# Performance work log

Hardware: AMD Instinct MI355X
Metric: run time of the kernel (lower is better)

The kernel has to match this reference:

```python
import jax, jax.numpy as jnp
import numpy as np

B, T = 2, 512
D, H, DFF = 1024, 16, 4096
V, CSL = 32000, 16
NL, NDL = 4, 2
MAXLEN = 1024
DH = D // H


def generate_ar_mask(L, csl):
    m = np.zeros((2 * L, 2 * L), dtype=bool)
    for i in range(L):
        m[:i] = True
        m[L + (i // csl) * csl: L + i] = True
    return jnp.asarray(m)


def generate_block_ntp_mask(L, csl):
    m = np.zeros((2 * L, 2 * L), dtype=bool)
    for c in range(L // csl):
        if c - 1 >= 0:
            m[:(c - 1) * csl] = True
        m[L + c * csl: L + (c + 1) * csl] = True
    return jnp.asarray(m)


def layernorm(x, g, b, eps=1e-5):
    mu = x.mean(-1, keepdims=True)
    var = x.var(-1, keepdims=True)
    return (x - mu) / jnp.sqrt(var + eps) * g + b


def block(x, mask, p):
    ln1g, ln1b, wqkv, bqkv, wo, bo, ln2g, ln2b, w1, b1, w2, b2 = p
    h = layernorm(x, ln1g, ln1b)
    qkv = h @ wqkv + bqkv                       # [B,S,3D]
    q, k, v = jnp.split(qkv, 3, axis=-1)
    bs, S, _ = x.shape
    q = q.reshape(bs, S, H, DH).transpose(0, 2, 1, 3)
    k = k.reshape(bs, S, H, DH).transpose(0, 2, 1, 3)
    v = v.reshape(bs, S, H, DH).transpose(0, 2, 1, 3)
    scores = jnp.einsum('bhqd,bhkd->bhqk', q, k) / jnp.sqrt(jnp.asarray(DH, x.dtype))
    scores = jnp.where(mask, scores, jnp.asarray(-1e9, x.dtype))
    attn = jax.nn.softmax(scores, axis=-1)
    o = jnp.einsum('bhqk,bhkd->bhqd', attn, v)
    o = o.transpose(0, 2, 1, 3).reshape(bs, S, D)
    x = x + (o @ wo + bo)
    h = layernorm(x, ln2g, ln2b)
    return x + (jax.nn.gelu(h @ w1 + b1, approximate=False) @ w2 + b2)


def setup_inputs():
    key = jax.random.key(0)
    ks = jax.random.split(key, 6)

    def pstack(k, n):
        kk = jax.random.split(k, 4)
        return dict(
            ln1g=jnp.ones((n, D)), ln1b=jnp.zeros((n, D)),
            wqkv=0.02 * jax.random.normal(kk[0], (n, D, 3 * D)), bqkv=jnp.zeros((n, 3 * D)),
            wo=0.02 * jax.random.normal(kk[1], (n, D, D)), bo=jnp.zeros((n, D)),
            ln2g=jnp.ones((n, D)), ln2b=jnp.zeros((n, D)),
            w1=0.02 * jax.random.normal(kk[2], (n, D, DFF)), b1=jnp.zeros((n, DFF)),
            w2=0.02 * jax.random.normal(kk[3], (n, DFF, D)), b2=jnp.zeros((n, D)))

    body = pstack(ks[0], NL)
    dec = pstack(ks[1], NDL)
    inp = {
        'tok_ids': jax.random.randint(ks[2], (B, T), 0, V),
        'tok_emb': 0.02 * jax.random.normal(ks[3], (V, D)),
        'pos_emb': 0.02 * jax.random.normal(ks[4], (MAXLEN, D)),
        'mask_tokens': 0.02 * jax.random.normal(ks[5], (1, CSL, D)),
    }
    for kname, vv in body.items():
        inp['b_' + kname] = vv
    for kname, vv in dec.items():
        inp['d_' + kname] = vv
    return inp


def reference(tok_ids, tok_emb, pos_emb, mask_tokens,
              b_ln1g, b_ln1b, b_wqkv, b_bqkv, b_wo, b_bo, b_ln2g, b_ln2b, b_w1, b_b1, b_w2, b_b2,
              d_ln1g, d_ln1b, d_wqkv, d_bqkv, d_wo, d_bo, d_ln2g, d_ln2b, d_w1, d_b1, d_w2, d_b2):
    Bq, Tq = tok_ids.shape
    pos = jnp.tile(jnp.arange(Tq), 2)            # pos ids repeated for both halves
    emb_pos = pos_emb[pos]                       # [2T, D], broadcast over batch
    mask_ids = jnp.tile(mask_tokens, (Bq, Tq // CSL, 1))
    x = jnp.concatenate([tok_emb[tok_ids], mask_ids], axis=1) + emb_pos[None]

    body_mask = generate_block_ntp_mask(Tq, CSL)
    bp = (b_ln1g, b_ln1b, b_wqkv, b_bqkv, b_wo, b_bo, b_ln2g, b_ln2b, b_w1, b_b1, b_w2, b_b2)
    for i in range(NL):
        x = block(x, body_mask, tuple(p[i] for p in bp))

    ar_mask = generate_ar_mask(Tq, CSL)
    dp = (d_ln1g, d_ln1b, d_wqkv, d_bqkv, d_wo, d_bo, d_ln2g, d_ln2b, d_w1, d_b1, d_w2, d_b2)
    for i in range(NDL):
        x = block(x, ar_mask, tuple(p[i] for p in dp))

    logits = (x @ tok_emb.T)[:, Tq + 1:, :]      # [B, T-1, V]
    tgt = tok_ids[:, :-1].reshape(-1)
    logits = logits.reshape(-1, V)
    logp = jax.nn.log_softmax(logits, axis=-1)
    loss = -jnp.take_along_axis(logp, tgt[:, None], axis=1).mean()
    return loss
```

## Files before the change

kernel.cpp:

```cpp
#include <hip/hip_runtime.h>
#include <hip/hip_bf16.h>
#include <math.h>

#define DD   1024
#define HHN  16
#define DHD  64
#define DFFN 4096
#define VV   32000
#define BBN  2
#define TTN  512
#define SSN  1024
#define NRN  2048

typedef __attribute__((ext_vector_type(8))) short short8;
typedef __attribute__((ext_vector_type(4))) float f32x4;

enum : long {
    LSTR    = 12582912,
    OFF_QKV = 0,
    OFF_WO  = 3145728,
    OFF_W1  = 4194304,
    OFF_W2  = 8388608
};

struct P24 { const float* p[24]; };

__device__ __forceinline__ unsigned short f2bf(float f) {
    __hip_bfloat16 h = __float2bfloat16(f);
    return __builtin_bit_cast(unsigned short, h);
}
__device__ __forceinline__ float bf2f(unsigned short u) {
    return __bfloat162float(__builtin_bit_cast(__hip_bfloat16, u));
}

__device__ __forceinline__ void glds16(const void* g, void* l) {
    __builtin_amdgcn_global_load_lds(
        (const __attribute__((address_space(1))) void*)g,
        (__attribute__((address_space(3))) void*)l,
        16, 0, 0);
}

__device__ __forceinline__ float blockReduceSum(float v) {
    __shared__ float sh[4];
    #pragma unroll
    for (int o = 1; o < 64; o <<= 1) v += __shfl_xor(v, o, 64);
    int lane = threadIdx.x & 63, wv = threadIdx.x >> 6;
    __syncthreads();
    if (lane == 0) sh[wv] = v;
    __syncthreads();
    return sh[0] + sh[1] + sh[2] + sh[3];
}

__global__ __launch_bounds__(256) void prep_k(P24 wp, unsigned short* __restrict__ wbf,
                                              const int* __restrict__ tok,
                                              const float* __restrict__ temb,
                                              const float* __restrict__ pemb,
                                              const float* __restrict__ mtok,
                                              float* __restrict__ x) {
    __shared__ __align__(16) unsigned short Lb[256 * 72];
    const int id = blockIdx.x;
    const int t = threadIdx.x;

    if (id < 4608) {
        int seg, base, K, N;
        long woff;
        if (id < 1152)      { seg = 0; base = 0;    K = DD;   N = 3 * DD; woff = OFF_QKV; }
        else if (id < 1536) { seg = 1; base = 1152; K = DD;   N = DD;     woff = OFF_WO;  }
        else if (id < 3072) { seg = 2; base = 1536; K = DD;   N = DFFN;   woff = OFF_W1;  }
        else                { seg = 3; base = 3072; K = DFFN; N = DD;     woff = OFF_W2;  }
        const int rid = id - base;
        const int tpl = (K / 256) * (N / 64);
        const int lz = rid / tpl, t2 = rid % tpl;
        const int nt = N / 64;
        const int n0 = (t2 % nt) * 64, k0 = (t2 / nt) * 256;
        const float* w = wp.p[seg * 6 + lz];
        unsigned short* wt = wbf + (size_t)lz * LSTR + woff;

        #pragma unroll
        for (int p = 0; p < 2; p++) {
            const int k = p * 128 + (t >> 1);
            const int nch = (t & 1) * 32;
            const int g = ((k >> 6) & 3) << 4;
            const float* src = w + (size_t)(k0 + k) * N + n0 + nch;
            __align__(16) unsigned short tmp[32];
            #pragma unroll
            for (int i = 0; i < 8; i++) {
                float4 f = ((const float4*)src)[i];
                tmp[i * 4 + 0] = f2bf(f.x); tmp[i * 4 + 1] = f2bf(f.y);
                tmp[i * 4 + 2] = f2bf(f.z); tmp[i * 4 + 3] = f2bf(f.w);
            }
            #pragma unroll
            for (int i = 0; i < 4; i++)
                *(int4*)&Lb[k * 72 + ((nch + i * 8) ^ g)] = *(const int4*)&tmp[i * 8];
        }
        __syncthreads();
        {
            const int rp  = t >> 3;
            const int sub = t & 7;
            const int kcg = sub & 3, kh = sub >> 2;
            const int colx = (2 * rp) ^ (kcg << 4);
            const int kb = kcg * 64 + kh * 32;
            __align__(16) unsigned short tA[32], tB[32];
            #pragma unroll
            for (int i = 0; i < 32; i++) {
                unsigned int v = *(const unsigned int*)&Lb[(kb + i) * 72 + colx];
                tA[i] = (unsigned short)(v & 0xffff);
                tB[i] = (unsigned short)(v >> 16);
            }
            unsigned short* d0 = wt + (size_t)(n0 + 2 * rp) * K + k0 + kb;
            unsigned short* d1 = d0 + K;
            #pragma unroll
            for (int i = 0; i < 4; i++) {
                ((int4*)d0)[i] = ((const int4*)tA)[i];
                ((int4*)d1)[i] = ((const int4*)tB)[i];
            }
        }
    } else {
        const int row = id - 4608;
        const int b = row >> 10, s = row & 1023;
        const int d = t * 4;
        const float* src;
        const float* pe;
        if (s < TTN) {
            int tid2 = tok[b * TTN + s];
            src = temb + (size_t)tid2 * DD + d;
            pe  = pemb + (size_t)s * DD + d;
        } else {
            int sm = s - TTN;
            src = mtok + (size_t)(sm & 15) * DD + d;
            pe  = pemb + (size_t)sm * DD + d;
        }
        float4 v = *(const float4*)src;
        float4 p = *(const float4*)pe;
        v.x += p.x; v.y += p.y; v.z += p.z; v.w += p.w;
        *(float4*)(x + (size_t)row * DD + d) = v;
    }
}

__global__ __launch_bounds__(256) void ln_k(const float* __restrict__ x,
                                            const float* __restrict__ g,
                                            const float* __restrict__ b,
                                            unsigned short* __restrict__ out) {
    int row = blockIdx.x;
    int d = threadIdx.x * 4;
    const float4 v = *(const float4*)(x + (size_t)row * DD + d);
    float s  = v.x + v.y + v.z + v.w;
    float ss = v.x * v.x + v.y * v.y + v.z * v.z + v.w * v.w;
    s  = blockReduceSum(s);
    ss = blockReduceSum(ss);
    float mu  = s * (1.0f / DD);
    float var = ss * (1.0f / DD) - mu * mu;
    float inv = rsqrtf(var + 1e-5f);
    const float4 gg = *(const float4*)(g + d);
    const float4 bb = *(const float4*)(b + d);
    ushort4 o;
    o.x = f2bf((v.x - mu) * inv * gg.x + bb.x);
    o.y = f2bf((v.y - mu) * inv * gg.y + bb.y);
    o.z = f2bf((v.z - mu) * inv * gg.z + bb.z);
    o.w = f2bf((v.w - mu) * inv * gg.w + bb.w);
    *(ushort4*)(out + (size_t)row * DD + d) = o;
}

__global__ __launch_bounds__(256) void conv_k(const float* __restrict__ w,
                                              unsigned short* __restrict__ o, long n) {
    long i = ((long)blockIdx.x * 256 + threadIdx.x) * 8;
    if (i >= n) return;
    float4 a = *(const float4*)(w + i);
    float4 b = *(const float4*)(w + i + 4);
    __align__(16) unsigned short tmp[8];
    tmp[0] = f2bf(a.x); tmp[1] = f2bf(a.y); tmp[2] = f2bf(a.z); tmp[3] = f2bf(a.w);
    tmp[4] = f2bf(b.x); tmp[5] = f2bf(b.y); tmp[6] = f2bf(b.z); tmp[7] = f2bf(b.w);
    *(int4*)(o + i) = *(const int4*)tmp;
}

__global__ __launch_bounds__(256, 4) void flash_k(
    const unsigned short* __restrict__ qkvb,
    unsigned short* __restrict__ o,
    int mtype) {
    __shared__ __align__(16) unsigned short Qs[64][72];
    __shared__ __align__(16) unsigned short Ks[64][72];
    __shared__ __align__(16) unsigned short Vs[64][72];
    __shared__ __align__(16) unsigned short Ps[64][72];
    __shared__ float vcol[64];

    const int blk = blockIdx.x;
    const int bh = blk >> 4, qt = blk & 15;
    const int b = bh >> 4, h = bh & 15;
    const int t = threadIdx.x;
    const int lane = t & 63;
    const int w = t >> 6;
    const int fr = lane & 15;
    const int g8 = (lane >> 4) * 8;
    const int g4 = (lane >> 4) * 4;

    {
        const int r = t >> 2, c0 = (t & 3) * 16;
        const unsigned short* src =
            qkvb + (size_t)(b * SSN + qt * 64 + r) * 3072 + h * 64 + c0;
        *(int4*)&Qs[r][c0]     = *(const int4*)(src);
        *(int4*)&Qs[r][c0 + 8] = *(const int4*)(src + 8);
    }
    __syncthreads();
    short8 aq[2];
    #pragma unroll
    for (int kk = 0; kk < 2; kk++)
        aq[kk] = *(const short8*)&Qs[w * 16 + fr][kk * 32 + g8];

    float mrun[4], lrun[4];
    f32x4 accO[4] = {};
    #pragma unroll
    for (int j = 0; j < 4; j++) { mrun[j] = -1e30f; lrun[j] = 0.f; }

    float vacc[16];
    #pragma unroll
    for (int j = 0; j < 16; j++) vacc[j] = 0.f;

    const unsigned short* kbase = qkvb + (size_t)(b * SSN) * 3072 + DD + h * 64;
    const unsigned short* vbase = qkvb + (size_t)(b * SSN) * 3072 + 2 * DD + h * 64;
    const int d0 = w * 16;

    for (int kt = 0; kt < 16; kt++) {
        __syncthreads();
        {
            const int r = t >> 2, c0 = (t & 3) * 16;
            const unsigned short* src = kbase + (size_t)(kt * 64 + r) * 3072 + c0;
            *(int4*)&Ks[r][c0]     = *(const int4*)(src);
            *(int4*)&Ks[r][c0 + 8] = *(const int4*)(src + 8);
        }
        {
            const unsigned short* src = vbase + (size_t)(kt * 64 + lane) * 3072 + d0;
            int4 q0 = *(const int4*)(src);
            int4 q1 = *(const int4*)(src + 8);
            const unsigned short* u = (const unsigned short*)&q0;
            #pragma unroll
            for (int j = 0; j < 8; j++) {
                Vs[d0 + j][lane] = u[j];
                vacc[j] += bf2f(u[j]);
            }
            const unsigned short* u2 = (const unsigned short*)&q1;
            #pragma unroll
            for (int j = 0; j < 8; j++) {
                Vs[d0 + 8 + j][lane] = u2[j];
                vacc[8 + j] += bf2f(u2[j]);
            }
        }
        __syncthreads();

        f32x4 a2[4] = {};
        #pragma unroll
        for (int n = 0; n < 4; n++) {
            short8 bk0 = *(const short8*)&Ks[n * 16 + fr][g8];
            short8 bk1 = *(const short8*)&Ks[n * 16 + fr][32 + g8];
            a2[n] = __builtin_amdgcn_mfma_f32_16x16x32_bf16(aq[0], bk0, a2[n], 0, 0, 0);
            a2[n] = __builtin_amdgcn_mfma_f32_16x16x32_bf16(aq[1], bk1, a2[n], 0, 0, 0);
        }
        #pragma unroll
        for (int j = 0; j < 4; j++) {
            float tm = fmaxf(fmaxf(a2[0][j], a2[1][j]), fmaxf(a2[2][j], a2[3][j]));
            tm *= 0.125f;
            #pragma unroll
            for (int o2 = 1; o2 < 16; o2 <<= 1) tm = fmaxf(tm, __shfl_xor(tm, o2, 64));
            const float mn = fmaxf(mrun[j], tm);
            const float alpha = __expf(mrun[j] - mn);
            mrun[j] = mn;
            float rs = 0.f;
            #pragma unroll
            for (int n = 0; n < 4; n++) {
                float pv = __expf(a2[n][j] * 0.125f - mn);
                rs += pv;
                Ps[w * 16 + g4 + j][n * 16 + fr] = f2bf(pv);
            }
            #pragma unroll
            for (int o2 = 1; o2 < 16; o2 <<= 1) rs += __shfl_xor(rs, o2, 64);
            lrun[j] = lrun[j] * alpha + rs;
            #pragma unroll
            for (int nd = 0; nd < 4; nd++) accO[nd][j] *= alpha;
        }
        #pragma unroll
        for (int kk = 0; kk < 2; kk++) {
            short8 pa = *(const short8*)&Ps[w * 16 + fr][kk * 32 + g8];
            #pragma unroll
            for (int nd = 0; nd < 4; nd++) {
                short8 vb = *(const short8*)&Vs[nd * 16 + fr][kk * 32 + g8];
                accO[nd] = __builtin_amdgcn_mfma_f32_16x16x32_bf16(pa, vb, accO[nd], 0, 0, 0);
            }
        }
    }

    #pragma unroll
    for (int j = 0; j < 16; j++) {
        float vs = vacc[j];
        #pragma unroll
        for (int o2 = 1; o2 < 64; o2 <<= 1) vs += __shfl_xor(vs, o2, 64);
        if (lane == j) vcol[d0 + j] = vs;
    }
    __syncthreads();

    #pragma unroll
    for (int nd = 0; nd < 4; nd++)
        #pragma unroll
        for (int j = 0; j < 4; j++) {
            const int row = qt * 64 + w * 16 + g4 + j;
            const int col = nd * 16 + fr;
            bool uni;
            if (mtype == 0) uni = (row >= 480 && row < 512);
            else            uni = (row == 511) || (row >= 512 && (row & 15) == 15);
            float val;
            if (uni) val = vcol[col] * (1.0f / 1024.0f);
            else     val = accO[nd][j] / lrun[j];
            o[(size_t)(b * SSN + row) * DD + h * 64 + col] = f2bf(val);
        }
}

template <bool DOLN>
__global__ __launch_bounds__(256) void rln_k(const float* __restrict__ pp,
                                             const float* __restrict__ bias,
                                             float* __restrict__ x,
                                             const float* __restrict__ g,
                                             const float* __restrict__ b,
                                             unsigned short* __restrict__ xb,
                                             unsigned short* __restrict__ xl) {
    const int row = blockIdx.x;
    const int d = threadIdx.x * 4;
    const size_t off = (size_t)row * DD + d;
    float4 v = *(const float4*)(x + off);
    #pragma unroll
    for (int sl = 0; sl < 4; sl++) {
        float4 p = *(const float4*)(pp + (size_t)sl * NRN * DD + off);
        v.x += p.x; v.y += p.y; v.z += p.z; v.w += p.w;
    }
    const float4 bv = *(const float4*)(bias + d);
    v.x += bv.x; v.y += bv.y; v.z += bv.z; v.w += bv.w;
    *(float4*)(x + off) = v;
    if (DOLN) {
        float s  = v.x + v.y + v.z + v.w;
        float ss = v.x * v.x + v.y * v.y + v.z * v.z + v.w * v.w;
        s  = blockReduceSum(s);
        ss = blockReduceSum(ss);
        float mu  = s * (1.0f / DD);
        float var = ss * (1.0f / DD) - mu * mu;
        float inv = rsqrtf(var + 1e-5f);
        const float4 gg = *(const float4*)(g + d);
        const float4 bb = *(const float4*)(b + d);
        ushort4 ov;
        ov.x = f2bf((v.x - mu) * inv * gg.x + bb.x);
        ov.y = f2bf((v.y - mu) * inv * gg.y + bb.y);
        ov.z = f2bf((v.z - mu) * inv * gg.z + bb.z);
        ov.w = f2bf((v.w - mu) * inv * gg.w + bb.w);
        *(ushort4*)(xb + off) = ov;
    } else {
        const int s = row & 1023;
        if (s >= 513) {
            const int xr = (row >> 10) * 511 + (s - 513);
            ushort4 ov;
            ov.x = f2bf(v.x); ov.y = f2bf(v.y); ov.z = f2bf(v.z); ov.w = f2bf(v.w);
            *(ushort4*)(xl + (size_t)xr * DD + d) = ov;
        }
    }
}

__global__ __launch_bounds__(256) void loss_row2_k(const float2* __restrict__ part,
                                                   const float* __restrict__ tgtlog,
                                                   float* __restrict__ rowloss) {
    const int r = blockIdx.x;
    const int t = threadIdx.x;
    float mx = -1e30f, s = 0.f;
    for (int i = t; i < 500; i += 256) {
        float2 p = part[(size_t)r * 500 + i];
        float m2 = fmaxf(mx, p.x);
        s = s * __expf(mx - m2) + p.y * __expf(p.x - m2);
        mx = m2;
    }
    #pragma unroll
    for (int o2 = 1; o2 < 64; o2 <<= 1) {
        float om = __shfl_xor(mx, o2, 64);
        float os = __shfl_xor(s, o2, 64);
        float m2 = fmaxf(mx, om);
        s = s * __expf(mx - m2) + os * __expf(om - m2);
        mx = m2;
    }
    __shared__ float shm[4], shs[4];
    int lane = t & 63, wv = t >> 6;
    if (lane == 0) { shm[wv] = mx; shs[wv] = s; }
    __syncthreads();
    if (t == 0) {
        float M = fmaxf(fmaxf(shm[0], shm[1]), fmaxf(shm[2], shm[3]));
        float S = shs[0] * __expf(shm[0] - M) + shs[1] * __expf(shm[1] - M)
                + shs[2] * __expf(shm[2] - M) + shs[3] * __expf(shm[3] - M);
        rowloss[r] = (logf(S) + M) - tgtlog[r];
    }
}

__global__ __launch_bounds__(256) void loss_final_k(const float* __restrict__ rowloss,
                                                    float* __restrict__ out) {
    int t = threadIdx.x;
    float s = 0.f;
    for (int i = t; i < 1022; i += 256) s += rowloss[i];
    s = blockReduceSum(s);
    if (t == 0) out[0] = s * (1.0f / 1022.0f);
}

template <int EPI, int KSPLIT, int BM>
__global__ __launch_bounds__(256) void gemm_k(
    const unsigned short* __restrict__ A, long lda,
    const unsigned short* __restrict__ Bt, long ldb,
    void* __restrict__ Cp, long ldc,
    const float* __restrict__ bias,
    int MT, int K, long kstr) {
    constexpr int MFRAG = BM / 32;
    __shared__ __align__(16) unsigned short As[2][BM][32];
    __shared__ __align__(16) unsigned short Bs[2][128][32];

    const int nwg = gridDim.x;
    const int q = nwg >> 3, r = nwg & 7;
    const int xcd = blockIdx.x & 7, lin = blockIdx.x >> 3;
    const int wg = (xcd < r ? xcd * (q + 1) : r * (q + 1) + (xcd - r) * q) + lin;
    const int tiles = nwg / KSPLIT;
    const int ks = wg / tiles;
    const int rem = wg % tiles;
    const int brow = (rem % MT) * BM;
    const int bcol = (rem / MT) * 128;
    const int Kl = K / KSPLIT;

    const int t = threadIdx.x;
    const int lane = t & 63;
    const int w = t >> 6;
    const int fr = lane & 15;
    const int g8 = (lane >> 4) * 8;

    const int sc = (lane & 3) * 8;
    const int srB = w * 32 + (lane >> 2);
    const unsigned short* bP0 = Bt + (size_t)(bcol + srB) * ldb + ks * Kl + sc;
    const unsigned short* bP1 = bP0 + (size_t)16 * ldb;
    const int srA = (BM == 128 ? w * 32 : w * 16) + (lane >> 2);
    const unsigned short* aP0 = A + (size_t)(brow + srA) * lda + ks * Kl + sc;
    const unsigned short* aP1 = aP0 + (size_t)16 * lda;

    f32x4 acc[MFRAG][4] = {};
    const int nsteps = Kl >> 5;

    auto stage = [&](int buf) {
        if constexpr (BM == 128) {
            glds16(aP0, &As[buf][w * 32][0]);
            glds16(aP1, &As[buf][w * 32 + 16][0]);
        } else {
            glds16(aP0, &As[buf][w * 16][0]);
        }
        glds16(bP0, &Bs[buf][w * 32][0]);
        glds16(bP1, &Bs[buf][w * 32 + 16][0]);
        aP0 += 32; aP1 += 32; bP0 += 32; bP1 += 32;
    };

    stage(0);
    asm volatile("s_waitcnt vmcnt(0)");
    __syncthreads();

    const int wrB = (w >> 1) * (BM / 2);
    int cur = 0;
    for (int s2 = 1; s2 < nsteps; ++s2) {
        const int nb = cur ^ 1;
        stage(nb);

        short8 af[MFRAG], bf[4];
        #pragma unroll
        for (int m = 0; m < MFRAG; m++)
            af[m] = *(const short8*)&As[cur][wrB + m * 16 + fr][g8];
        #pragma unroll
        for (int n = 0; n < 4; n++)
            bf[n] = *(const short8*)&Bs[cur][(w & 1) * 64 + n * 16 + fr][g8];
        #pragma unroll
        for (int m = 0; m < MFRAG; m++)
            #pragma unroll
            for (int n = 0; n < 4; n++)
                acc[m][n] = __builtin_amdgcn_mfma_f32_16x16x32_bf16(af[m], bf[n], acc[m][n], 0, 0, 0);
        __syncthreads();
        cur = nb;
    }
    {
        short8 af[MFRAG], bf[4];
        #pragma unroll
        for (int m = 0; m < MFRAG; m++)
            af[m] = *(const short8*)&As[cur][wrB + m * 16 + fr][g8];
        #pragma unroll
        for (int n = 0; n < 4; n++)
            bf[n] = *(const short8*)&Bs[cur][(w & 1) * 64 + n * 16 + fr][g8];
        #pragma unroll
        for (int m = 0; m < MFRAG; m++)
            #pragma unroll
            for (int n = 0; n < 4; n++)
                acc[m][n] = __builtin_amdgcn_mfma_f32_16x16x32_bf16(af[m], bf[n], acc[m][n], 0, 0, 0);
    }

    const int wc = (w & 1) * 64;
    const int g4 = (lane >> 4) * 4;
    #pragma unroll
    for (int n = 0; n < 4; n++) {
        const int col = bcol + wc + n * 16 + fr;
        const float bv = bias ? bias[col] : 0.f;
        #pragma unroll
        for (int m = 0; m < MFRAG; m++) {
            #pragma unroll
            for (int j = 0; j < 4; j++) {
                const int row = brow + wrB + m * 16 + g4 + j;
                float v = acc[m][n][j] + bv;
                const size_t ci = (size_t)row * ldc + col;
                if (EPI == 0) {
                    ((float*)Cp)[ci] = v;
                } else if (EPI == 1) {
                    ((unsigned short*)Cp)[ci] = f2bf(v);
                } else if (EPI == 2) {
                    float gl = 0.5f * v * (1.0f + erff(v * 0.70710678118654752f));
                    ((unsigned short*)Cp)[ci] = f2bf(gl);
                } else if (EPI == 3) {
                    ((float*)Cp)[ci] += v;
                } else {
                    ((float*)Cp)[(size_t)ks * kstr + ci] = v;
                }
            }
        }
    }
}

__global__ __launch_bounds__(256) void gemm_lse_k(
    const unsigned short* __restrict__ A,
    const unsigned short* __restrict__ Bt,
    float2* __restrict__ part,
    float* __restrict__ tgtlog,
    const int* __restrict__ tok) {
    __shared__ __align__(16) unsigned short As[2][128][32];
    __shared__ __align__(16) unsigned short Bs[2][128][32];

    const int nwg = gridDim.x;
    const int q = nwg >> 3, r = nwg & 7;
    const int xcd = blockIdx.x & 7, lin = blockIdx.x >> 3;
    const int wg = (xcd < r ? xcd * (q + 1) : r * (q + 1) + (xcd - r) * q) + lin;
    const int MT = 8;
    const int brow = (wg % MT) * 128;
    const int bcol = (wg / MT) * 128;

    const int t = threadIdx.x;
    const int lane = t & 63;
    const int w = t >> 6;
    const int fr = lane & 15;
    const int g8 = (lane >> 4) * 8;

    const int sr = w * 32 + (lane >> 2);
    const int sc = (lane & 3) * 8;
    const unsigned short* aP0 = A + (size_t)(brow + sr) * DD + sc;
    const unsigned short* aP1 = aP0 + (size_t)16 * DD;
    const unsigned short* bP0 = Bt + (size_t)(bcol + sr) * DD + sc;
    const unsigned short* bP1 = bP0 + (size_t)16 * DD;

    f32x4 acc[4][4] = {};

    glds16(aP0, &As[0][w * 32][0]);
    glds16(aP1, &As[0][w * 32 + 16][0]);
    glds16(bP0, &Bs[0][w * 32][0]);
    glds16(bP1, &Bs[0][w * 32 + 16][0]);
    aP0 += 32; aP1 += 32; bP0 += 32; bP1 += 32;
    asm volatile("s_waitcnt vmcnt(0)");
    __syncthreads();

    int cur = 0;
    for (int s2 = 1; s2 < 32; ++s2) {
        const int nb = cur ^ 1;
        glds16(aP0, &As[nb][w * 32][0]);
        glds16(aP1, &As[nb][w * 32 + 16][0]);
        glds16(bP0, &Bs[nb][w * 32][0]);
        glds16(bP1, &Bs[nb][w * 32 + 16][0]);
        aP0 += 32; aP1 += 32; bP0 += 32; bP1 += 32;

        short8 af[4], bf[4];
        #pragma unroll
        for (int m = 0; m < 4; m++)
            af[m] = *(const short8*)&As[cur][(w >> 1) * 64 + m * 16 + fr][g8];
        #pragma unroll
        for (int n = 0; n < 4; n++)
            bf[n] = *(const short8*)&Bs[cur][(w & 1) * 64 + n * 16 + fr][g8];
        #pragma unroll
        for (int m = 0; m < 4; m++)
            #pragma unroll
            for (int n = 0; n < 4; n++)
                acc[m][n] = __builtin_amdgcn_mfma_f32_16x16x32_bf16(af[m], bf[n], acc[m][n], 0, 0, 0);
        __syncthreads();
        cur = nb;
    }
    {
        short8 af[4], bf[4];
        #pragma unroll
        for (int m = 0; m < 4; m++)
            af[m] = *(const short8*)&As[cur][(w >> 1) * 64 + m * 16 + fr][g8];
        #pragma unroll
        for (int n = 0; n < 4; n++)
            bf[n] = *(const short8*)&Bs[cur][(w & 1) * 64 + n * 16 + fr][g8];
        #pragma unroll
        for (int m = 0; m < 4; m++)
            #pragma unroll
            for (int n = 0; n < 4; n++)
                acc[m][n] = __builtin_amdgcn_mfma_f32_16x16x32_bf16(af[m], bf[n], acc[m][n], 0, 0, 0);
    }

    const int wr = (w >> 1) * 64;
    const int wc = (w & 1) * 64;
    const int g4 = (lane >> 4) * 4;
    const int ct2 = (bcol >> 7) * 2 + (w & 1);
    #pragma unroll
    for (int m = 0; m < 4; m++) {
        #pragma unroll
        for (int j = 0; j < 4; j++) {
            const int grow = brow + wr + m * 16 + g4 + j;
            const float v0 = acc[m][0][j], v1 = acc[m][1][j];
            const float v2 = acc[m][2][j], v3 = acc[m][3][j];
            float mx = fmaxf(fmaxf(v0, v1), fmaxf(v2, v3));
            #pragma unroll
            for (int o2 = 1; o2 < 16; o2 <<= 1) mx = fmaxf(mx, __shfl_xor(mx, o2, 64));
            float s = __expf(v0 - mx) + __expf(v1 - mx) + __expf(v2 - mx) + __expf(v3 - mx);
            #pragma unroll
            for (int o2 = 1; o2 < 16; o2 <<= 1) s += __shfl_xor(s, o2, 64);
            if (fr == 0) {
                float2 p; p.x = mx; p.y = s;
                part[(size_t)grow * 500 + ct2] = p;
            }
            int tgtc = -1;
            if (grow < 511) tgtc = tok[grow];
            else if (grow >= 511 && grow < 1022) tgtc = tok[512 + grow - 511];
            const int cl = tgtc - (bcol + wc);
            if (tgtc >= 0 && cl >= 0 && cl < 64 && (cl & 15) == fr) {
                const float vv[4] = {v0, v1, v2, v3};
                tgtlog[grow] = vv[cl >> 4];
            }
        }
    }
}

extern "C" void kernel_launch(void* const* d_in, const int* in_sizes, int n_in,
                              void* d_out, int out_size, void* d_ws, size_t ws_size,
                              hipStream_t stream) {
    const int*   tok  = (const int*)d_in[0];
    const float* temb = (const float*)d_in[1];
    const float* pemb = (const float*)d_in[2];
    const float* mtok = (const float*)d_in[3];
    const float* W[24];
    for (int i = 0; i < 24; i++) W[i] = (const float*)d_in[4 + i];

    char* ws = (char*)d_ws;
    float*          x      = (float*)(ws + 0);
    unsigned short* xb     = (unsigned short*)(ws + 8388608);
    unsigned short* qkvb   = (unsigned short*)(ws + 12582912);
    unsigned short* o      = (unsigned short*)(ws + 25165824);
    unsigned short* g      = (unsigned short*)(ws + 29360128);
    float*          pp     = (float*)(ws + 46137344);
    unsigned short* wbf    = (unsigned short*)(ws + 79691776);
    unsigned short* tembb  = (unsigned short*)(ws + 79691776);
    float2*         part   = (float2*)(ws + 145227776);
    float*          tgtlog = (float*)(ws + 149327872);
    unsigned short* xl     = (unsigned short*)(ws + 230686720);
    float*          rowloss= (float*)(ws + 232783872);

    P24 wp;
    for (int l = 0; l < 6; l++) {
        const int grp = (l < 4) ? 0 : 1;
        const int li  = (l < 4) ? l : l - 4;
        const float* const* P = W + grp * 12;
        wp.p[0 + l]  = P[2]  + (size_t)li * DD * 3 * DD;
        wp.p[6 + l]  = P[4]  + (size_t)li * DD * DD;
        wp.p[12 + l] = P[8]  + (size_t)li * DD * DFFN;
        wp.p[18 + l] = P[10] + (size_t)li * DFFN * DD;
    }
    prep_k<<<4608 + 2048, 256, 0, stream>>>(wp, wbf, tok, temb, pemb, mtok, x);

    for (int l = 0; l < 6; l++) {
        const int grp = (l < 4) ? 0 : 1;
        const int li  = (l < 4) ? l : l - 4;
        const float* const* P = W + grp * 12;
        const float* ln1g = P[0] + (size_t)li * DD;
        const float* ln1b = P[1] + (size_t)li * DD;
        const float* bqkv = P[3] + (size_t)li * 3 * DD;
        const float* bo   = P[5] + (size_t)li * DD;
        const float* ln2g = P[6] + (size_t)li * DD;
        const float* ln2b = P[7] + (size_t)li * DD;
        const float* b1   = P[9] + (size_t)li * DFFN;
        const float* b2   = P[11] + (size_t)li * DD;
        unsigned short* wl = wbf + (size_t)l * LSTR;

        if (l == 0) ln_k<<<NRN, 256, 0, stream>>>(x, ln1g, ln1b, xb);
        gemm_k<1, 1, 64><<<32 * 24, 256, 0, stream>>>(xb, DD, wl + OFF_QKV, DD,
                                                      qkvb, 3 * DD, bqkv, 32, DD, 0);
        flash_k<<<512, 256, 0, stream>>>(qkvb, o, grp);
        gemm_k<3, 1, 64><<<32 * 8, 256, 0, stream>>>(o, DD, wl + OFF_WO, DD,
                                                     x, DD, bo, 32, DD, 0);

        ln_k<<<NRN, 256, 0, stream>>>(x, ln2g, ln2b, xb);
        gemm_k<2, 1, 128><<<16 * 32, 256, 0, stream>>>(xb, DD, wl + OFF_W1, DD,
                                                       g, DFFN, b1, 16, DD, 0);
        gemm_k<4, 4, 128><<<16 * 8 * 4, 256, 0, stream>>>(g, DFFN, wl + OFF_W2, DFFN,
                                                          pp, DD, nullptr, 16, DFFN,
                                                          (long)NRN * DD);
        if (l < 5) {
            const int l2 = l + 1;
            const int grp2 = (l2 < 4) ? 0 : 1;
            const int li2  = (l2 < 4) ? l2 : l2 - 4;
            const float* const* P2 = W + grp2 * 12;
            rln_k<true><<<NRN, 256, 0, stream>>>(pp, b2, x,
                                                 P2[0] + (size_t)li2 * DD,
                                                 P2[1] + (size_t)li2 * DD, xb, nullptr);
        } else {
            rln_k<false><<<NRN, 256, 0, stream>>>(pp, b2, x, nullptr, nullptr, nullptr, xl);
        }
    }

    conv_k<<<16000, 256, 0, stream>>>(temb, tembb, (long)VV * DD);
    gemm_lse_k<<<2000, 256, 0, stream>>>(xl, tembb, part, tgtlog, tok);
    loss_row2_k<<<1022, 256, 0, stream>>>(part, tgtlog, rowloss);
    loss_final_k<<<1, 256, 0, stream>>>(rowloss, (float*)d_out);
}
```

Measured before the change: 1.495 ms.

## Reduce split-K W2 partials with atomics into residual and reshape weight conversion loads

The W2 split-K GEMM now atomically adds each K-slice's result (with bias only on slice 0) straight into the fp32 residual x, instead of writing four partial buffers that a separate residual-plus-layernorm kernel summed. The following kernel becomes a plain layernorm, and the last layer uses a small kernel that only extracts and converts the logit rows. The weight-prep kernel also switches to coalesced float4 loads of 16 rows per pass. This removes the partial-buffer writes and reads, but adds atomic traffic and makes the summation order nondeterministic.

```diff
diff --git a/kernel.cpp b/kernel.cpp
--- a/kernel.cpp
+++ b/kernel.cpp
@@ -76,22 +76,18 @@
         const float* w = wp.p[seg * 6 + lz];
         unsigned short* wt = wbf + (size_t)lz * LSTR + woff;
 
-        #pragma unroll
-        for (int p = 0; p < 2; p++) {
-            const int k = p * 128 + (t >> 1);
-            const int nch = (t & 1) * 32;
-            const int g = ((k >> 6) & 3) << 4;
-            const float* src = w + (size_t)(k0 + k) * N + n0 + nch;
-            __align__(16) unsigned short tmp[32];
-            #pragma unroll
-            for (int i = 0; i < 8; i++) {
-                float4 f = ((const float4*)src)[i];
-                tmp[i * 4 + 0] = f2bf(f.x); tmp[i * 4 + 1] = f2bf(f.y);
-                tmp[i * 4 + 2] = f2bf(f.z); tmp[i * 4 + 3] = f2bf(f.w);
-            }
-            #pragma unroll
-            for (int i = 0; i < 4; i++)
-                *(int4*)&Lb[k * 72 + ((nch + i * 8) ^ g)] = *(const int4*)&tmp[i * 8];
+        const int kr = t >> 4;
+        const int nc = (t & 15) * 4;
+        #pragma unroll
+        for (int p = 0; p < 16; p++) {
+            const int k = p * 16 + kr;
+            const int g = (k >> 6) << 4;
+            float4 f = *(const float4*)(w + (size_t)(k0 + k) * N + n0 + nc);
+            __align__(8) unsigned short tmp[4];
+            tmp[0] = f2bf(f.x); tmp[1] = f2bf(f.y);
+            tmp[2] = f2bf(f.z); tmp[3] = f2bf(f.w);
+            *(unsigned long long*)&Lb[k * 72 + (nc ^ g)] =
+                *(const unsigned long long*)tmp;
         }
         __syncthreads();
         {
@@ -312,51 +308,17 @@
         }
 }
 
-template <bool DOLN>
-__global__ __launch_bounds__(256) void rln_k(const float* __restrict__ pp,
-                                             const float* __restrict__ bias,
-                                             float* __restrict__ x,
-                                             const float* __restrict__ g,
-                                             const float* __restrict__ b,
-                                             unsigned short* __restrict__ xb,
+__global__ __launch_bounds__(256) void gxl_k(const float* __restrict__ x,
                                              unsigned short* __restrict__ xl) {
-    const int row = blockIdx.x;
-    const int d = threadIdx.x * 4;
-    const size_t off = (size_t)row * DD + d;
-    float4 v = *(const float4*)(x + off);
-    #pragma unroll
-    for (int sl = 0; sl < 4; sl++) {
-        float4 p = *(const float4*)(pp + (size_t)sl * NRN * DD + off);
-        v.x += p.x; v.y += p.y; v.z += p.z; v.w += p.w;
-    }
-    const float4 bv = *(const float4*)(bias + d);
-    v.x += bv.x; v.y += bv.y; v.z += bv.z; v.w += bv.w;
-    *(float4*)(x + off) = v;
-    if (DOLN) {
-        float s  = v.x + v.y + v.z + v.w;
-        float ss = v.x * v.x + v.y * v.y + v.z * v.z + v.w * v.w;
-        s  = blockReduceSum(s);
-        ss = blockReduceSum(ss);
-        float mu  = s * (1.0f / DD);
-        float var = ss * (1.0f / DD) - mu * mu;
-        float inv = rsqrtf(var + 1e-5f);
-        const float4 gg = *(const float4*)(g + d);
-        const float4 bb = *(const float4*)(b + d);
-        ushort4 ov;
-        ov.x = f2bf((v.x - mu) * inv * gg.x + bb.x);
-        ov.y = f2bf((v.y - mu) * inv * gg.y + bb.y);
-        ov.z = f2bf((v.z - mu) * inv * gg.z + bb.z);
-        ov.w = f2bf((v.w - mu) * inv * gg.w + bb.w);
-        *(ushort4*)(xb + off) = ov;
-    } else {
-        const int s = row & 1023;
-        if (s >= 513) {
-            const int xr = (row >> 10) * 511 + (s - 513);
-            ushort4 ov;
-            ov.x = f2bf(v.x); ov.y = f2bf(v.y); ov.z = f2bf(v.z); ov.w = f2bf(v.w);
-            *(ushort4*)(xl + (size_t)xr * DD + d) = ov;
-        }
-    }
+    int r = blockIdx.x;
+    int d = threadIdx.x * 4;
+    ushort4 o = {0, 0, 0, 0};
+    if (r < 1022) {
+        int b = r / 511, i = r % 511;
+        float4 v = *(const float4*)(x + (size_t)(b * SSN + 513 + i) * DD + d);
+        o.x = f2bf(v.x); o.y = f2bf(v.y); o.z = f2bf(v.z); o.w = f2bf(v.w);
+    }
+    *(ushort4*)(xl + (size_t)r * DD + d) = o;
 }
 
 __global__ __launch_bounds__(256) void loss_row2_k(const float2* __restrict__ part,
@@ -496,7 +458,7 @@
     #pragma unroll
     for (int n = 0; n < 4; n++) {
         const int col = bcol + wc + n * 16 + fr;
-        const float bv = bias ? bias[col] : 0.f;
+        const float bv = (bias && (KSPLIT == 1 || ks == 0)) ? bias[col] : 0.f;
         #pragma unroll
         for (int m = 0; m < MFRAG; m++) {
             #pragma unroll
@@ -514,7 +476,7 @@
                 } else if (EPI == 3) {
                     ((float*)Cp)[ci] += v;
                 } else {
-                    ((float*)Cp)[(size_t)ks * kstr + ci] = v;
+                    atomicAdd(&((float*)Cp)[ci], v);
                 }
             }
         }
@@ -649,7 +611,6 @@
     unsigned short* qkvb   = (unsigned short*)(ws + 12582912);
     unsigned short* o      = (unsigned short*)(ws + 25165824);
     unsigned short* g      = (unsigned short*)(ws + 29360128);
-    float*          pp     = (float*)(ws + 46137344);
     unsigned short* wbf    = (unsigned short*)(ws + 79691776);
     unsigned short* tembb  = (unsigned short*)(ws + 79691776);
     float2*         part   = (float2*)(ws + 145227776);
@@ -694,18 +655,16 @@
         gemm_k<2, 1, 128><<<16 * 32, 256, 0, stream>>>(xb, DD, wl + OFF_W1, DD,
                                                        g, DFFN, b1, 16, DD, 0);
         gemm_k<4, 4, 128><<<16 * 8 * 4, 256, 0, stream>>>(g, DFFN, wl + OFF_W2, DFFN,
-                                                          pp, DD, nullptr, 16, DFFN,
-                                                          (long)NRN * DD);
+                                                          x, DD, b2, 16, DFFN, 0);
         if (l < 5) {
             const int l2 = l + 1;
             const int grp2 = (l2 < 4) ? 0 : 1;
             const int li2  = (l2 < 4) ? l2 : l2 - 4;
             const float* const* P2 = W + grp2 * 12;
-            rln_k<true><<<NRN, 256, 0, stream>>>(pp, b2, x,
-                                                 P2[0] + (size_t)li2 * DD,
-                                                 P2[1] + (size_t)li2 * DD, xb, nullptr);
+            ln_k<<<NRN, 256, 0, stream>>>(x, P2[0] + (size_t)li2 * DD,
+                                          P2[1] + (size_t)li2 * DD, xb);
         } else {
-            rln_k<false><<<NRN, 256, 0, stream>>>(pp, b2, x, nullptr, nullptr, nullptr, xl);
+            gxl_k<<<1024, 256, 0, stream>>>(x, xl);
         }
     }
 
```

Measured after the change: 1.546 ms. 3.4% more time.
